# Kernel optimization log

Hardware: AMD Instinct MI355X
Metric: run time of the kernel (lower is better)

Reference implementation:

```python
import math
import jax, jax.numpy as jnp
import numpy as np

N_HEAD = 16
NUM_BUCKETS = 32
MAX_DISTANCE = 2048
NEG_INF = -1e9  # finite stand-in for -inf in masked_fill; rows always have >=1 unmasked entry


def _relative_position_bucket(relative_position, num_buckets=NUM_BUCKETS, max_distance=MAX_DISTANCE):
    # causal (bidirectional=False) T5 bucketing
    rp = -jnp.minimum(relative_position, 0)  # nonneg distances
    max_exact = num_buckets // 2
    is_small = rp < max_exact
    rp_safe = jnp.maximum(rp, 1).astype(jnp.float32)
    large = max_exact + (
        jnp.log(rp_safe / max_exact) / math.log(max_distance / max_exact) * (num_buckets - max_exact)
    ).astype(jnp.int32)
    large = jnp.minimum(large, num_buckets - 1)
    return jnp.where(is_small, rp, large)


def t5_bias(rel_table, T):
    ctx = jnp.arange(T)[:, None]
    mem = jnp.arange(T)[None, :]
    buckets = _relative_position_bucket(mem - ctx)        # [T, T]
    bias = rel_table[buckets]                              # [T, T, H]
    return jnp.transpose(bias, (2, 0, 1))                  # [H, T, T]


def setup_inputs() -> dict:
    key = jax.random.key(0)
    k1, k2, k3, k4 = jax.random.split(key, 4)
    B, T, C = 2, 2048, 1024
    x = jax.random.normal(k1, (B, T, C), dtype=jnp.float32)
    w_qkv = jax.random.normal(k2, (C, 3 * C), dtype=jnp.float32) * (1.0 / math.sqrt(C))
    w_proj = jax.random.normal(k3, (C, C), dtype=jnp.float32) * (1.0 / math.sqrt(C))
    rel_table = jax.random.normal(k4, (NUM_BUCKETS, N_HEAD), dtype=jnp.float32) * 0.02
    return {"x": x, "w_qkv": w_qkv, "w_proj": w_proj, "rel_table": rel_table}


def reference(x, w_qkv, w_proj, rel_table):
    B, T, C = x.shape
    H = N_HEAD
    d = C // H
    qkv = x @ w_qkv                                        # [B, T, 3C]
    q, k, v = jnp.split(qkv, 3, axis=-1)
    q = q.reshape(B, T, H, d).transpose(0, 2, 1, 3)        # [B, H, T, d]
    k = k.reshape(B, T, H, d).transpose(0, 2, 1, 3)
    v = v.reshape(B, T, H, d).transpose(0, 2, 1, 3)

    bias = t5_bias(rel_table, T)                           # [H, T, T]
    causal = jnp.tril(jnp.ones((T, T), dtype=bool))
    bias = jnp.where(causal[None], bias, NEG_INF)          # masked_fill(-inf) on bias

    scores = jnp.einsum("bhqd,bhkd->bhqk", q, k) * (1.0 / math.sqrt(d))
    scores = scores + bias[None]                           # broadcast over batch
    att = jax.nn.softmax(scores, axis=-1)
    y = jnp.einsum("bhqk,bhkd->bhqd", att, v)              # [B, H, T, d]
    y = y.transpose(0, 2, 1, 3).reshape(B, T, C)
    return y @ w_proj
```

## Files before the change

kernel.cpp:

```cpp
#include <hip/hip_runtime.h>
#include <hip/hip_bf16.h>
#include <cstdint>
#include <cstddef>

#define B_  2
#define T_  2048
#define C_  1024
#define H_  16
#define D_  64
#define NEG_INF_ -1e9f

typedef short bf16x8 __attribute__((ext_vector_type(8)));
typedef float f32x4  __attribute__((ext_vector_type(4)));

__device__ __forceinline__ short f2bf(float f) {
  union { float f; unsigned u; } x; x.f = f;
  unsigned r = (x.u + 0x7fffu + ((x.u >> 16) & 1u)) >> 16;
  return (short)r;
}

__device__ __forceinline__ float bf2f(short s) {
  union { float f; unsigned u; } x;
  x.u = ((unsigned)(unsigned short)s) << 16;
  return x.f;
}

__device__ __forceinline__ void gload16(const void* g, void* l) {
  __builtin_amdgcn_global_load_lds(
      (const __attribute__((address_space(1))) unsigned int*)g,
      (__attribute__((address_space(3))) unsigned int*)l, 16, 0, 0);
}

__global__ __launch_bounds__(256) void cvt_bf16(const float* __restrict__ in,
                                                short* __restrict__ out, int n4) {
  int i = blockIdx.x * 256 + threadIdx.x;
  if (i < n4) {
    float4 v = ((const float4*)in)[i];
    short4 o;
    o.x = f2bf(v.x); o.y = f2bf(v.y); o.z = f2bf(v.z); o.w = f2bf(v.w);
    ((short4*)out)[i] = o;
  }
}

__global__ __launch_bounds__(256) void transpose_cvt(const float* __restrict__ in,
                                                     short* __restrict__ out,
                                                     int R, int C) {
  __shared__ float tile[32][33];
  int gx = blockIdx.x * 32, gy = blockIdx.y * 32;
  int tx = threadIdx.x, ty = threadIdx.y;
#pragma unroll
  for (int i = 0; i < 4; ++i)
    tile[ty + i * 8][tx] = in[(size_t)(gy + ty + i * 8) * C + gx + tx];
  __syncthreads();
#pragma unroll
  for (int i = 0; i < 4; ++i)
    out[(size_t)(gx + ty + i * 8) * R + gy + tx] = f2bf(tile[tx][ty + i * 8]);
}

__global__ __launch_bounds__(256) void bias_table(const float* __restrict__ rel_table,
                                                  float* __restrict__ btab) {
  int idx = blockIdx.x * 256 + threadIdx.x;
  if (idx >= H_ * T_) return;
  int dist = idx & (T_ - 1);
  int h = idx >> 11;
  int bucket;
  if (dist < 16) {
    bucket = dist;
  } else {
    float rp = (float)dist;
    int large = 16 + (int)(logf(rp * (1.0f / 16.0f)) * (1.0f / logf(128.0f)) * 16.0f);
    bucket = large < 31 ? large : 31;
  }
  btab[idx] = rel_table[bucket * H_ + h];
}

template <int MODE>
__global__ __launch_bounds__(256) void gemm_bt128(
    const short* __restrict__ A, const short* __restrict__ Bt,
    int M, int N, int K,
    short* __restrict__ q_out, short* __restrict__ k_out,
    short* __restrict__ vT_out, float* __restrict__ f_out) {
  __shared__ alignas(16) short As[128 * 64];
  __shared__ alignas(16) short Bs[128 * 64];
  const int tid = threadIdx.x;
  const int w = tid >> 6, lane = tid & 63;
  const int g = lane >> 4, l16 = lane & 15;
  const int wr = w >> 1, wc = w & 1;
  const int m0 = blockIdx.y * 128, n0 = blockIdx.x * 128;

  const char* Ag = (const char*)(A + (size_t)m0 * K);
  const char* Bg = (const char*)(Bt + (size_t)n0 * K);
  char* AsB = (char*)As;
  char* BsB = (char*)Bs;

  int goff[4];
#pragma unroll
  for (int i = 0; i < 4; ++i) {
    int o = i * 256 + tid;
    int row = o >> 3, ch = o & 7;
    goff[i] = row * (K * 2) + ((ch ^ (row & 7)) << 4);
  }

  f32x4 acc[4][4] = {};

  const int nkt = K >> 6;
  for (int kt = 0; kt < nkt; ++kt) {
    __syncthreads();
    const int kbyte = kt << 7;
#pragma unroll
    for (int i = 0; i < 4; ++i)
      gload16(Ag + goff[i] + kbyte, AsB + i * 4096 + w * 1024);
#pragma unroll
    for (int i = 0; i < 4; ++i)
      gload16(Bg + goff[i] + kbyte, BsB + i * 4096 + w * 1024);
    __syncthreads();
#pragma unroll
    for (int kk = 0; kk < 2; ++kk) {
      bf16x8 af[4], bff[4];
#pragma unroll
      for (int m = 0; m < 4; ++m) {
        int r = wr * 64 + m * 16 + l16;
        int off = (r * 128 + kk * 64 + g * 16) ^ ((r & 7) << 4);
        af[m] = *(const bf16x8*)(AsB + off);
      }
#pragma unroll
      for (int n = 0; n < 4; ++n) {
        int c = wc * 64 + n * 16 + l16;
        int off = (c * 128 + kk * 64 + g * 16) ^ ((c & 7) << 4);
        bff[n] = *(const bf16x8*)(BsB + off);
      }
#pragma unroll
      for (int m = 0; m < 4; ++m)
#pragma unroll
        for (int n = 0; n < 4; ++n)
          acc[m][n] = __builtin_amdgcn_mfma_f32_16x16x32_bf16(af[m], bff[n], acc[m][n], 0, 0, 0);
    }
  }

#pragma unroll
  for (int m = 0; m < 4; ++m) {
#pragma unroll
    for (int n = 0; n < 4; ++n) {
      const int colg = n0 + wc * 64 + n * 16 + l16;
#pragma unroll
      for (int r = 0; r < 4; ++r) {
        const int rowg = m0 + wr * 64 + m * 16 + g * 4 + r;
        float v = acc[m][n][r];
        if (MODE == 1) {
          f_out[(size_t)rowg * N + colg] = v;
        } else {
          int part = colg >> 10;
          int within = colg & 1023;
          int h = within >> 6, dd = within & 63;
          int b = rowg >> 11, t = rowg & (T_ - 1);
          size_t bh = (size_t)(b * H_ + h);
          if (part == 0)
            q_out[(bh * T_ + t) * D_ + dd] = f2bf(v * 0.125f);
          else if (part == 1)
            k_out[(bh * T_ + t) * D_ + dd] = f2bf(v);
          else
            vT_out[(bh * D_ + dd) * T_ + t] = f2bf(v);
        }
      }
    }
  }
}

__global__ __launch_bounds__(256) void attn64(
    const short* __restrict__ qb, const short* __restrict__ kb,
    const short* __restrict__ vTb, const float* __restrict__ bias_tab,
    short* __restrict__ o1, short* __restrict__ o2, float* __restrict__ mlb) {
  __shared__ alignas(16) short Ks[2][64 * 64];
  __shared__ alignas(16) short Vs[64 * 64];
  __shared__ alignas(16) short Ps[4][16 * 64];
  __shared__ float biasw[2][2][128];
  const int tid = threadIdx.x;
  const int w = tid >> 6, lane = tid & 63;
  const int g = lane >> 4, l16 = lane & 15;
  const int bh = blockIdx.y;
  const int h = bh & (H_ - 1);
  const int b = bh >> 4;
  const int j = blockIdx.x;
  const int s = blockIdx.z;
  const int qlo = j, qhi = 31 - j;
  const int q0l = qlo * 64, q0h = qhi * 64;

  const char* kbase = (const char*)(kb + (size_t)bh * T_ * D_);
  const char* vbase = (const char*)(vTb + (size_t)bh * D_ * T_);
  const float* btab = bias_tab + h * T_;

  bf16x8 qfl[2], qfh[2];
  {
    const short* qrl = qb + ((size_t)bh * T_ + q0l + w * 16 + l16) * D_;
    qfl[0] = *(const bf16x8*)(qrl + g * 8);
    qfl[1] = *(const bf16x8*)(qrl + 32 + g * 8);
    const short* qrh = qb + ((size_t)bh * T_ + q0h + w * 16 + l16) * D_;
    qfh[0] = *(const bf16x8*)(qrh + g * 8);
    qfh[1] = *(const bf16x8*)(qrh + 32 + g * 8);
  }

  f32x4 accl[4] = {}, acch[4] = {};
  float mlo[4], llo[4], mhi[4], lhi[4];
#pragma unroll
  for (int r = 0; r < 4; ++r) { mlo[r] = mhi[r] = -1e30f; llo[r] = lhi[r] = 0.f; }

  char* PsB = (char*)&Ps[w][0];

  int krow[2], kch[2];
#pragma unroll
  for (int i = 0; i < 2; ++i) {
    int o = i * 256 + tid;
    krow[i] = o >> 3;
    kch[i] = (o & 7) ^ (krow[i] & 7);
  }

  auto stageK = [&](int buf, int t) {
    const int kv0 = t * 64;
    char* KsB = (char*)&Ks[buf][0];
#pragma unroll
    for (int i = 0; i < 2; ++i)
      gload16(kbase + (size_t)(kv0 + krow[i]) * 128 + kch[i] * 16,
              KsB + i * 4096 + w * 1024);
  };
  auto stageV = [&](int t) {
    const int kv0 = t * 64;
    char* VsB = (char*)Vs;
#pragma unroll
    for (int i = 0; i < 2; ++i)
      gload16(vbase + (size_t)krow[i] * (T_ * 2) + kv0 * 2 + kch[i] * 16,
              VsB + i * 4096 + w * 1024);
  };
  auto biasLoad = [&](int t) -> float {
    int i = tid & 127;
    int q0x = (tid >= 128) ? q0h : q0l;
    int d = q0x - t * 64 - 63 + i;
    return (d >= 0 && d < T_) ? btab[d] : NEG_INF_;
  };

  auto computeTile = [&](const char* KsB, const float* bw, const bf16x8* qf,
                         f32x4* acc, float* mrun, float* lrun,
                         bool dosync, bool drain2) {
    f32x4 sreg[4];
    __builtin_amdgcn_s_setprio(1);
#pragma unroll
    for (int n = 0; n < 4; ++n) {
      int kvrow = n * 16 + l16;
      int off0 = (kvrow * 128 + g * 16) ^ ((kvrow & 7) << 4);
      int off1 = (kvrow * 128 + 64 + g * 16) ^ ((kvrow & 7) << 4);
      bf16x8 k0 = *(const bf16x8*)(KsB + off0);
      bf16x8 k1 = *(const bf16x8*)(KsB + off1);
      f32x4 z = {};
      z = __builtin_amdgcn_mfma_f32_16x16x32_bf16(qf[0], k0, z, 0, 0, 0);
      z = __builtin_amdgcn_mfma_f32_16x16x32_bf16(qf[1], k1, z, 0, 0, 0);
      sreg[n] = z;
    }
    __builtin_amdgcn_s_setprio(0);

    float sv[4][4];
    float tmax[4] = {-1e30f, -1e30f, -1e30f, -1e30f};
#pragma unroll
    for (int n = 0; n < 4; ++n) {
#pragma unroll
      for (int r = 0; r < 4; ++r) {
        int idx = 63 + w * 16 + g * 4 + r - n * 16 - l16;
        float val = sreg[n][r] + bw[idx];
        sv[n][r] = val;
        tmax[r] = fmaxf(tmax[r], val);
      }
    }
#pragma unroll
    for (int r = 0; r < 4; ++r) {
      float v = tmax[r];
      v = fmaxf(v, __shfl_xor(v, 1));
      v = fmaxf(v, __shfl_xor(v, 2));
      v = fmaxf(v, __shfl_xor(v, 4));
      v = fmaxf(v, __shfl_xor(v, 8));
      tmax[r] = v;
    }

    bool nogrow = true;
#pragma unroll
    for (int r = 0; r < 4; ++r) nogrow &= (tmax[r] <= mrun[r] + 8.0f);
    if (!__all(nogrow)) {
#pragma unroll
      for (int r = 0; r < 4; ++r) {
        float mnew = fmaxf(mrun[r], tmax[r]);
        float scale = __expf(mrun[r] - mnew);
        mrun[r] = mnew;
        lrun[r] *= scale;
#pragma unroll
        for (int dn = 0; dn < 4; ++dn) acc[dn][r] *= scale;
      }
    }

#pragma unroll
    for (int r = 0; r < 4; ++r) {
      float su = 0.f;
#pragma unroll
      for (int n = 0; n < 4; ++n) {
        float p = __expf(sv[n][r] - mrun[r]);
        su += p;
        int row = g * 4 + r, col = n * 16 + l16;
        int off = (row * 128 + col * 2) ^ ((row & 7) << 4);
        *(short*)(PsB + off) = f2bf(p);
      }
      lrun[r] += su;
    }

    if (dosync) {
      if (drain2) {
        asm volatile("s_waitcnt vmcnt(2)" ::: "memory");
      } else {
        asm volatile("s_waitcnt vmcnt(0)" ::: "memory");
      }
      __builtin_amdgcn_s_barrier();
      __builtin_amdgcn_sched_barrier(0);
    }

    const char* VsB = (const char*)Vs;
    bf16x8 pf[2];
    {
      int o0 = (l16 * 128 + g * 16) ^ ((l16 & 7) << 4);
      int o1 = (l16 * 128 + 64 + g * 16) ^ ((l16 & 7) << 4);
      pf[0] = *(const bf16x8*)(PsB + o0);
      pf[1] = *(const bf16x8*)(PsB + o1);
    }
    __builtin_amdgcn_s_setprio(1);
#pragma unroll
    for (int dn = 0; dn < 4; ++dn) {
      int drow = dn * 16 + l16;
      int o0 = (drow * 128 + g * 16) ^ ((drow & 7) << 4);
      int o1 = (drow * 128 + 64 + g * 16) ^ ((drow & 7) << 4);
      bf16x8 v0 = *(const bf16x8*)(VsB + o0);
      bf16x8 v1 = *(const bf16x8*)(VsB + o1);
      acc[dn] = __builtin_amdgcn_mfma_f32_16x16x32_bf16(pf[0], v0, acc[dn], 0, 0, 0);
      acc[dn] = __builtin_amdgcn_mfma_f32_16x16x32_bf16(pf[1], v1, acc[dn], 0, 0, 0);
    }
    __builtin_amdgcn_s_setprio(0);
  };

  stageK(0, s);
  {
    float bv = biasLoad(s);
    biasw[0][tid >> 7][tid & 127] = bv;
  }
  __syncthreads();

  int cur = 0;
  for (int t = s; t <= qhi; t += 2) {
    const int nxt = cur ^ 1;
    const bool hasnext = (t + 2 <= qhi);
    float bvn = 0.f;
    if (hasnext) bvn = biasLoad(t + 2);
    stageV(t);
    if (hasnext) stageK(nxt, t + 2);
    const char* KsB = (const char*)&Ks[cur][0];
    bool first = true;
    if (t <= qlo) {
      computeTile(KsB, &biasw[cur][0][0], qfl, accl, mlo, llo, true, hasnext);
      first = false;
    }
    computeTile(KsB, &biasw[cur][1][0], qfh, acch, mhi, lhi, first, hasnext);
    if (hasnext) biasw[nxt][tid >> 7][tid & 127] = bvn;
    __syncthreads();
    cur = nxt;
  }

  short* dst = (s == 0) ? o1 : o2;
  auto writeO = [&](int q0x, const f32x4* acc, const float* mrun, float* lrun) {
#pragma unroll
    for (int r = 0; r < 4; ++r) {
      float v = lrun[r];
      v += __shfl_xor(v, 1);
      v += __shfl_xor(v, 2);
      v += __shfl_xor(v, 4);
      v += __shfl_xor(v, 8);
      int qg = q0x + w * 16 + g * 4 + r;
      size_t ybase = ((size_t)b * T_ + qg) * C_ + h * D_;
#pragma unroll
      for (int dn = 0; dn < 4; ++dn)
        dst[ybase + dn * 16 + l16] = f2bf(acc[dn][r]);
      if (l16 == 0) {
        int idx = (((b * T_) + qg) * H_ + h) * 4 + s * 2;
        mlb[idx] = mrun[r];
        mlb[idx + 1] = v;
      }
    }
  };
  writeO(q0l, accl, mlo, llo);
  writeO(q0h, acch, mhi, lhi);
}

__global__ __launch_bounds__(256) void attn_merge(
    short* __restrict__ o1, const short* __restrict__ o2,
    const float* __restrict__ mlb) {
  int i = blockIdx.x * 256 + threadIdx.x;
  int row = i >> 7;
  int h = (i & 127) >> 3;
  float4 q = ((const float4*)mlb)[row * H_ + h];
  float m = fmaxf(q.x, q.z);
  float w0 = __expf(q.x - m), w1 = __expf(q.z - m);
  float inv = 1.0f / (w0 * q.y + w1 * q.w);
  bf16x8 a = ((const bf16x8*)o1)[i];
  bf16x8 bb = ((const bf16x8*)o2)[i];
  bf16x8 o;
#pragma unroll
  for (int e = 0; e < 8; ++e)
    o[e] = f2bf((w0 * bf2f(a[e]) + w1 * bf2f(bb[e])) * inv);
  ((bf16x8*)o1)[i] = o;
}

extern "C" void kernel_launch(void* const* d_in, const int* in_sizes, int n_in,
                              void* d_out, int out_size, void* d_ws, size_t ws_size,
                              hipStream_t stream) {
  const float* x = (const float*)d_in[0];
  const float* w_qkv = (const float*)d_in[1];
  const float* w_proj = (const float*)d_in[2];
  const float* rel_table = (const float*)d_in[3];
  float* out = (float*)d_out;

  const size_t MB = 1024 * 1024;
  char* ws = (char*)d_ws;
  short* xb     = (short*)(ws);
  short* wqkvT  = (short*)(ws + 8 * MB);
  short* wprojT = (short*)(ws + 14 * MB);
  short* qb     = (short*)(ws + 16 * MB);
  short* kbuf   = (short*)(ws + 24 * MB);
  short* vT     = (short*)(ws + 32 * MB);
  short* yb     = (short*)(ws + 40 * MB);
  float* btab   = (float*)(ws + 48 * MB);
  short* o2b    = (short*)(ws);
  float* mlb    = (float*)(ws + 9 * MB);

  cvt_bf16<<<4096, 256, 0, stream>>>(x, xb, (B_ * T_ * C_) / 4);
  dim3 tb(32, 8);
  transpose_cvt<<<dim3(96, 32), tb, 0, stream>>>(w_qkv, wqkvT, 1024, 3072);
  transpose_cvt<<<dim3(32, 32), tb, 0, stream>>>(w_proj, wprojT, 1024, 1024);
  bias_table<<<128, 256, 0, stream>>>(rel_table, btab);

  gemm_bt128<0><<<dim3(24, 32), 256, 0, stream>>>(xb, wqkvT, 4096, 3072, 1024,
                                                  qb, kbuf, vT, nullptr);
  attn64<<<dim3(16, 32, 2), 256, 0, stream>>>(qb, kbuf, vT, btab, yb, o2b, mlb);
  attn_merge<<<2048, 256, 0, stream>>>(yb, o2b, mlb);

  gemm_bt128<1><<<dim3(8, 32), 256, 0, stream>>>(yb, wprojT, 4096, 1024, 1024,
                                                 nullptr, nullptr, nullptr, out);
}
```

Measured before the change: 227.0 us.

## Use exp2 softmax, separate V transpose kernel, and 128x64 tiles for output projection

Folds log2(e) into the q scaling and the bias table so the softmax can use exp2 directly, and packs two probabilities per bf16 conversion instruction. The QKV GEMM now writes V row-major, and a new vtrans kernel transposes it through shared memory instead of the GEMM epilogue doing strided transposed stores. The output-projection GEMM switches to 128x64 tiles, doubling the block count to 512 to fill more CUs. The cost is an extra kernel launch and an extra pass over V in memory.

```diff
diff --git a/kernel.cpp b/kernel.cpp
--- a/kernel.cpp
+++ b/kernel.cpp
@@ -9,6 +9,7 @@
 #define H_  16
 #define D_  64
 #define NEG_INF_ -1e9f
+#define LOG2E_ 1.44269504f
 
 typedef short bf16x8 __attribute__((ext_vector_type(8)));
 typedef float f32x4  __attribute__((ext_vector_type(4)));
@@ -71,22 +72,24 @@
     int large = 16 + (int)(logf(rp * (1.0f / 16.0f)) * (1.0f / logf(128.0f)) * 16.0f);
     bucket = large < 31 ? large : 31;
   }
-  btab[idx] = rel_table[bucket * H_ + h];
-}
-
-template <int MODE>
-__global__ __launch_bounds__(256) void gemm_bt128(
+  btab[idx] = rel_table[bucket * H_ + h] * LOG2E_;
+}
+
+template <int MODE, int BN>
+__global__ __launch_bounds__(256) void gemm_bt(
     const short* __restrict__ A, const short* __restrict__ Bt,
     int M, int N, int K,
     short* __restrict__ q_out, short* __restrict__ k_out,
-    short* __restrict__ vT_out, float* __restrict__ f_out) {
+    short* __restrict__ v_out, float* __restrict__ f_out) {
   __shared__ alignas(16) short As[128 * 64];
-  __shared__ alignas(16) short Bs[128 * 64];
+  __shared__ alignas(16) short Bs[BN * 64];
   const int tid = threadIdx.x;
   const int w = tid >> 6, lane = tid & 63;
   const int g = lane >> 4, l16 = lane & 15;
-  const int wr = w >> 1, wc = w & 1;
-  const int m0 = blockIdx.y * 128, n0 = blockIdx.x * 128;
+  const int wrb = (BN == 128) ? (w >> 1) * 64 : w * 32;
+  const int wcb = (BN == 128) ? (w & 1) * 64 : 0;
+  const int MR = (BN == 128) ? 4 : 2;
+  const int m0 = blockIdx.y * 128, n0 = blockIdx.x * BN;
 
   const char* Ag = (const char*)(A + (size_t)m0 * K);
   const char* Bg = (const char*)(Bt + (size_t)n0 * K);
@@ -100,8 +103,9 @@
     int row = o >> 3, ch = o & 7;
     goff[i] = row * (K * 2) + ((ch ^ (row & 7)) << 4);
   }
-
-  f32x4 acc[4][4] = {};
+  const int NBI = (BN == 128) ? 4 : 2;
+
+  f32x4 acc[MR][4] = {};
 
   const int nkt = K >> 6;
   for (int kt = 0; kt < nkt; ++kt) {
@@ -111,26 +115,26 @@
     for (int i = 0; i < 4; ++i)
       gload16(Ag + goff[i] + kbyte, AsB + i * 4096 + w * 1024);
 #pragma unroll
-    for (int i = 0; i < 4; ++i)
+    for (int i = 0; i < NBI; ++i)
       gload16(Bg + goff[i] + kbyte, BsB + i * 4096 + w * 1024);
     __syncthreads();
 #pragma unroll
     for (int kk = 0; kk < 2; ++kk) {
-      bf16x8 af[4], bff[4];
-#pragma unroll
-      for (int m = 0; m < 4; ++m) {
-        int r = wr * 64 + m * 16 + l16;
+      bf16x8 af[MR], bff[4];
+#pragma unroll
+      for (int m = 0; m < MR; ++m) {
+        int r = wrb + m * 16 + l16;
         int off = (r * 128 + kk * 64 + g * 16) ^ ((r & 7) << 4);
         af[m] = *(const bf16x8*)(AsB + off);
       }
 #pragma unroll
       for (int n = 0; n < 4; ++n) {
-        int c = wc * 64 + n * 16 + l16;
+        int c = wcb + n * 16 + l16;
         int off = (c * 128 + kk * 64 + g * 16) ^ ((c & 7) << 4);
         bff[n] = *(const bf16x8*)(BsB + off);
       }
 #pragma unroll
-      for (int m = 0; m < 4; ++m)
+      for (int m = 0; m < MR; ++m)
 #pragma unroll
         for (int n = 0; n < 4; ++n)
           acc[m][n] = __builtin_amdgcn_mfma_f32_16x16x32_bf16(af[m], bff[n], acc[m][n], 0, 0, 0);
@@ -138,13 +142,13 @@
   }
 
 #pragma unroll
-  for (int m = 0; m < 4; ++m) {
+  for (int m = 0; m < MR; ++m) {
 #pragma unroll
     for (int n = 0; n < 4; ++n) {
-      const int colg = n0 + wc * 64 + n * 16 + l16;
+      const int colg = n0 + wcb + n * 16 + l16;
 #pragma unroll
       for (int r = 0; r < 4; ++r) {
-        const int rowg = m0 + wr * 64 + m * 16 + g * 4 + r;
+        const int rowg = m0 + wrb + m * 16 + g * 4 + r;
         float v = acc[m][n][r];
         if (MODE == 1) {
           f_out[(size_t)rowg * N + colg] = v;
@@ -155,14 +159,42 @@
           int b = rowg >> 11, t = rowg & (T_ - 1);
           size_t bh = (size_t)(b * H_ + h);
           if (part == 0)
-            q_out[(bh * T_ + t) * D_ + dd] = f2bf(v * 0.125f);
+            q_out[(bh * T_ + t) * D_ + dd] = f2bf(v * (0.125f * LOG2E_));
           else if (part == 1)
             k_out[(bh * T_ + t) * D_ + dd] = f2bf(v);
           else
-            vT_out[(bh * D_ + dd) * T_ + t] = f2bf(v);
+            v_out[(bh * T_ + t) * D_ + dd] = f2bf(v);
         }
       }
     }
+  }
+}
+
+__global__ __launch_bounds__(256) void vtrans(const short* __restrict__ vbuf,
+                                              short* __restrict__ vT) {
+  __shared__ short tile[64][65];
+  const int tid = threadIdx.x;
+  const int bh = blockIdx.y;
+  const int t0 = blockIdx.x * 64;
+  const short* src = vbuf + ((size_t)bh * T_ + t0) * D_;
+#pragma unroll
+  for (int i = 0; i < 2; ++i) {
+    int c = i * 256 + tid;
+    int tr = c >> 3, dc = (c & 7) * 8;
+    bf16x8 v = *(const bf16x8*)(src + tr * D_ + dc);
+#pragma unroll
+    for (int e = 0; e < 8; ++e) tile[tr][dc + e] = v[e];
+  }
+  __syncthreads();
+  short* dst = vT + (size_t)bh * D_ * T_ + t0;
+#pragma unroll
+  for (int i = 0; i < 2; ++i) {
+    int c = i * 256 + tid;
+    int d = c >> 3, oct = (c & 7) * 8;
+    bf16x8 o;
+#pragma unroll
+    for (int j = 0; j < 8; ++j) o[j] = tile[oct + j][d];
+    *(bf16x8*)(dst + (size_t)d * T_ + oct) = o;
   }
 }
 
@@ -280,12 +312,12 @@
 
     bool nogrow = true;
 #pragma unroll
-    for (int r = 0; r < 4; ++r) nogrow &= (tmax[r] <= mrun[r] + 8.0f);
+    for (int r = 0; r < 4; ++r) nogrow &= (tmax[r] <= mrun[r] + 11.5417f);
     if (!__all(nogrow)) {
 #pragma unroll
       for (int r = 0; r < 4; ++r) {
         float mnew = fmaxf(mrun[r], tmax[r]);
-        float scale = __expf(mrun[r] - mnew);
+        float scale = exp2f(mrun[r] - mnew);
         mrun[r] = mnew;
         lrun[r] *= scale;
 #pragma unroll
@@ -296,13 +328,17 @@
 #pragma unroll
     for (int r = 0; r < 4; ++r) {
       float su = 0.f;
-#pragma unroll
-      for (int n = 0; n < 4; ++n) {
-        float p = __expf(sv[n][r] - mrun[r]);
-        su += p;
-        int row = g * 4 + r, col = n * 16 + l16;
-        int off = (row * 128 + col * 2) ^ ((row & 7) << 4);
-        *(short*)(PsB + off) = f2bf(p);
+      const int rowoff = (g * 4 + r) * 128;
+      const int sw = ((g * 4 + r) & 7) << 4;
+#pragma unroll
+      for (int np = 0; np < 2; ++np) {
+        float p0 = exp2f(sv[2 * np][r] - mrun[r]);
+        float p1 = exp2f(sv[2 * np + 1][r] - mrun[r]);
+        su += p0 + p1;
+        unsigned pk;
+        asm("v_cvt_pk_bf16_f32 %0, %1, %2" : "=v"(pk) : "v"(p0), "v"(p1));
+        *(short*)(PsB + ((rowoff + (2 * np * 16 + l16) * 2) ^ sw)) = (short)pk;
+        *(short*)(PsB + ((rowoff + ((2 * np + 1) * 16 + l16) * 2) ^ sw)) = (short)(pk >> 16);
       }
       lrun[r] += su;
     }
@@ -399,7 +435,7 @@
   int h = (i & 127) >> 3;
   float4 q = ((const float4*)mlb)[row * H_ + h];
   float m = fmaxf(q.x, q.z);
-  float w0 = __expf(q.x - m), w1 = __expf(q.z - m);
+  float w0 = exp2f(q.x - m), w1 = exp2f(q.z - m);
   float inv = 1.0f / (w0 * q.y + w1 * q.w);
   bf16x8 a = ((const bf16x8*)o1)[i];
   bf16x8 bb = ((const bf16x8*)o2)[i];
@@ -426,11 +462,12 @@
   short* wprojT = (short*)(ws + 14 * MB);
   short* qb     = (short*)(ws + 16 * MB);
   short* kbuf   = (short*)(ws + 24 * MB);
-  short* vT     = (short*)(ws + 32 * MB);
-  short* yb     = (short*)(ws + 40 * MB);
+  short* vbuf   = (short*)(ws + 32 * MB);
+  short* vT     = (short*)(ws + 40 * MB);
   float* btab   = (float*)(ws + 48 * MB);
   short* o2b    = (short*)(ws);
   float* mlb    = (float*)(ws + 9 * MB);
+  short* o1b    = (short*)(ws + 32 * MB);
 
   cvt_bf16<<<4096, 256, 0, stream>>>(x, xb, (B_ * T_ * C_) / 4);
   dim3 tb(32, 8);
@@ -438,11 +475,13 @@
   transpose_cvt<<<dim3(32, 32), tb, 0, stream>>>(w_proj, wprojT, 1024, 1024);
   bias_table<<<128, 256, 0, stream>>>(rel_table, btab);
 
-  gemm_bt128<0><<<dim3(24, 32), 256, 0, stream>>>(xb, wqkvT, 4096, 3072, 1024,
-                                                  qb, kbuf, vT, nullptr);
-  attn64<<<dim3(16, 32, 2), 256, 0, stream>>>(qb, kbuf, vT, btab, yb, o2b, mlb);
-  attn_merge<<<2048, 256, 0, stream>>>(yb, o2b, mlb);
-
-  gemm_bt128<1><<<dim3(8, 32), 256, 0, stream>>>(yb, wprojT, 4096, 1024, 1024,
-                                                 nullptr, nullptr, nullptr, out);
-}
+  gemm_bt<0, 128><<<dim3(24, 32), 256, 0, stream>>>(xb, wqkvT, 4096, 3072, 1024,
+                                                    qb, kbuf, vbuf, nullptr);
+  vtrans<<<dim3(32, 32), 256, 0, stream>>>(vbuf, vT);
+
+  attn64<<<dim3(16, 32, 2), 256, 0, stream>>>(qb, kbuf, vT, btab, o1b, o2b, mlb);
+  attn_merge<<<2048, 256, 0, stream>>>(o1b, o2b, mlb);
+
+  gemm_bt<1, 64><<<dim3(16, 32), 256, 0, stream>>>(o1b, wprojT, 4096, 1024, 1024,
+                                                   nullptr, nullptr, nullptr, out);
+}
```

After: 220.9 us. 1.03x faster.
